# Optimization experiments

Hardware: AMD Instinct MI355X
Metric: run time of the kernel (lower is better)

The kernel has to match this reference:

```python
import jax, jax.numpy as jnp
import numpy as np

EPS = 1e-12  # matches torch F.normalize eps


def _l2norm(t):
    n = jnp.linalg.norm(t, axis=-1, keepdims=True)
    return t / jnp.maximum(n, EPS)


def setup_inputs() -> dict:
    key = jax.random.key(0)
    ks = jax.random.split(key, 10)
    B, N, C = 2, 2048, 384
    nH, hd = 12, 32
    inp = {
        "x": jax.random.normal(ks[0], (B, N, C), jnp.float32),
        "q_w": jax.random.normal(ks[1], (C, C), jnp.float32) * 0.02,
        "q_b": jax.random.normal(ks[2], (C,), jnp.float32) * 0.02,
        "kv_w": jax.random.normal(ks[3], (2 * C, C), jnp.float32) * 0.02,
        "kv_b": jax.random.normal(ks[4], (2 * C,), jnp.float32) * 0.02,
        "query_embedding": jax.random.normal(ks[5], (nH, 1, hd), jnp.float32) * 0.02,
        # init of temperature in torch: log(exp(1/0.24) - 1)
        "temperature": jnp.full((nH, 1, 1), float(np.log(np.exp(1.0 / 0.24) - 1.0)), jnp.float32),
        "pos_bias": jax.random.normal(ks[7], (nH, N), jnp.float32) * 0.0004,
        "proj_w": jax.random.normal(ks[8], (C, C), jnp.float32) * 0.02,
        "proj_b": jax.random.normal(ks[9], (C,), jnp.float32) * 0.02,
        "D": 8, "H": 16, "W": 16,
    }
    return inp


def reference(x, q_w, q_b, kv_w, kv_b, query_embedding, temperature, pos_bias, proj_w, proj_b, D, H, W):
    B, N, C = x.shape
    nH, hd = query_embedding.shape[0], query_embedding.shape[2]
    assert N == D * H * W
    # q projection -> [B, nH, N, hd], cosine-normalized
    q = (x @ q_w.T + q_b).reshape(B, N, nH, hd).transpose(0, 2, 1, 3)
    q = _l2norm(q)
    # additive query embedding, softplus temperature, seq-length (log N) scale
    scale = jax.nn.softplus(temperature) * jnp.float32(np.log(N))  # [nH,1,1]
    q = (q + query_embedding[None]) * scale[None]
    # kv projection
    kv = x @ kv_w.T + kv_b  # [B, N, 2C]
    k, v = kv[..., :C], kv[..., C:]
    k = _l2norm(k.reshape(B, N, nH, hd).transpose(0, 2, 1, 3))
    v = v.reshape(B, N, nH, hd).transpose(0, 2, 1, 3)
    # scores with per-head learned positional bias over keys
    attn = jnp.einsum("bhqd,bhkd->bhqk", q, k) + pos_bias[None, :, None, :]
    attn = jax.nn.softmax(attn, axis=-1)
    out = jnp.einsum("bhqk,bhkd->bhqd", attn, v)
    out = out.transpose(0, 2, 1, 3).reshape(B, N, C)
    return out @ proj_w.T + proj_b
```

## Files before the change

kernel.cpp:

```cpp
#include <hip/hip_runtime.h>

#define LOG2E 1.4426950408889634f

typedef __bf16 bf16x8 __attribute__((ext_vector_type(8)));
typedef short s16x4 __attribute__((ext_vector_type(4)));
typedef float f32x4 __attribute__((ext_vector_type(4)));

#define BB 2
#define NN 2048
#define CC 384
#define NH 12
#define HD 32
#define MROWS (BB * NN)

__device__ __forceinline__ unsigned short f2bf(float f) {
  __bf16 h = (__bf16)f;
  return __builtin_bit_cast(unsigned short, h);
}

__device__ __forceinline__ bf16x8 ldg_bf8(const unsigned short* p) {
  uint4 v = *reinterpret_cast<const uint4*>(p);
  return __builtin_bit_cast(bf16x8, v);
}

__device__ __forceinline__ float fexp2(float x) {
#if __has_builtin(__builtin_amdgcn_exp2f)
  return __builtin_amdgcn_exp2f(x);
#else
  return exp2f(x);
#endif
}

__device__ __forceinline__ s16x4 pack_bf4(float a, float b, float c, float d) {
#if __has_builtin(__builtin_amdgcn_cvt_pk_bf16_f32)
  auto lo = __builtin_amdgcn_cvt_pk_bf16_f32(a, b);
  auto hi = __builtin_amdgcn_cvt_pk_bf16_f32(c, d);
  uint2 u = {__builtin_bit_cast(unsigned int, lo),
             __builtin_bit_cast(unsigned int, hi)};
  return __builtin_bit_cast(s16x4, u);
#else
  s16x4 r = {(short)f2bf(a), (short)f2bf(b), (short)f2bf(c), (short)f2bf(d)};
  return r;
#endif
}

typedef __attribute__((address_space(1))) const void gas_void;
typedef __attribute__((address_space(3))) void las_void;
__device__ __forceinline__ void gload_lds16(const void* g, void* l) {
  __builtin_amdgcn_global_load_lds((gas_void*)(unsigned long long)g,
                                   (las_void*)(unsigned long long)l, 16, 0, 0);
}

__device__ __forceinline__ f32x4 mfma32(bf16x8 a, bf16x8 b, f32x4 c) {
  return __builtin_amdgcn_mfma_f32_16x16x32_bf16(a, b, c, 0, 0, 0);
}

__device__ __forceinline__ f32x4 mfma16(s16x4 a, s16x4 b, f32x4 c) {
#if defined(__HIP_DEVICE_COMPILE__)
#if __has_builtin(__builtin_amdgcn_mfma_f32_16x16x16bf16_1k)
  return __builtin_amdgcn_mfma_f32_16x16x16bf16_1k(a, b, c, 0, 0, 0);
#else
  asm volatile("v_mfma_f32_16x16x16_bf16 %0, %1, %2, %0"
               : "+v"(c) : "v"(a), "v"(b));
  return c;
#endif
#else
  return c;
#endif
}

__global__ __launch_bounds__(256) void prep_kernel(
    const float* __restrict__ x, const float* __restrict__ q_w,
    const float* __restrict__ kv_w, const float* __restrict__ proj_w,
    const float* __restrict__ pos_bias, unsigned short* __restrict__ xb,
    unsigned short* __restrict__ qwb, unsigned short* __restrict__ kvwb,
    unsigned short* __restrict__ pwb, float* __restrict__ bias2) {
  long i = (long)(blockIdx.x * 256 + threadIdx.x) * 8;
  auto cast8 = [&](const float* s, unsigned short* d, long off) {
    float4 a = *reinterpret_cast<const float4*>(s + off);
    float4 b = *reinterpret_cast<const float4*>(s + off + 4);
    s16x4 lo = pack_bf4(a.x, a.y, a.z, a.w);
    s16x4 hi = pack_bf4(b.x, b.y, b.z, b.w);
    uint2 l = __builtin_bit_cast(uint2, lo), h = __builtin_bit_cast(uint2, hi);
    uint4 o = {l.x, l.y, h.x, h.y};
    *reinterpret_cast<uint4*>(d + off) = o;
  };
  if (i < 1572864) { cast8(x, xb, i); return; }
  i -= 1572864;
  if (i < 147456) { cast8(q_w, qwb, i); return; }
  i -= 147456;
  if (i < 294912) { cast8(kv_w, kvwb, i); return; }
  i -= 294912;
  if (i < 147456) { cast8(proj_w, pwb, i); return; }
  i -= 147456;
  float4 a = *reinterpret_cast<const float4*>(pos_bias + i);
  float4 b = *reinterpret_cast<const float4*>(pos_bias + i + 4);
  a.x *= LOG2E; a.y *= LOG2E; a.z *= LOG2E; a.w *= LOG2E;
  b.x *= LOG2E; b.y *= LOG2E; b.z *= LOG2E; b.w *= LOG2E;
  *reinterpret_cast<float4*>(bias2 + i) = a;
  *reinterpret_cast<float4*>(bias2 + i + 4) = b;
}

__global__ __launch_bounds__(256, 4) void gemm_qkv_norm_kernel(
    const unsigned short* __restrict__ xb, const unsigned short* __restrict__ qwb,
    const unsigned short* __restrict__ kvwb, const float* __restrict__ q_b,
    const float* __restrict__ kv_b, const float* __restrict__ qe,
    const float* __restrict__ temperature, unsigned short* __restrict__ Qs,
    unsigned short* __restrict__ Kn, unsigned short* __restrict__ VT) {
  __shared__ alignas(16) char smem[2][20480];
  int wave = threadIdx.x >> 6, lane = threadIdx.x & 63;
  int c = lane & 15, quad = lane >> 4;
  int h = blockIdx.y;
  int m0b = blockIdx.x * 64;
  int cid = wave * 64 + lane;

  auto stage = [&](int buf, int kk) {
    char* base = smem[buf];
#pragma unroll
    for (int j = 0; j < 2; ++j) {
      int chunk = j * 256 + cid;
      int row = chunk >> 3, e = chunk & 7;
      gload_lds16(xb + (long)(m0b + row) * CC + kk + (e ^ (row & 7)) * 8,
                  base + j * 4096 + wave * 1024);
    }
#pragma unroll
    for (int j = 0; j < 3; ++j) {
      int chunk = j * 256 + cid;
      int row = chunk >> 3, e = chunk & 7;
      const unsigned short* src;
      if (row < 32)      src = qwb + (long)(h * 32 + row) * CC;
      else if (row < 64) src = kvwb + (long)(h * 32 + (row - 32)) * CC;
      else               src = kvwb + (long)(CC + h * 32 + (row - 64)) * CC;
      gload_lds16(src + kk + (e ^ (row & 7)) * 8,
                  base + 8192 + j * 4096 + wave * 1024);
    }
  };

  f32x4 acc[6] = {};
  auto compute = [&](int buf) {
    const char* base = smem[buf];
#pragma unroll
    for (int kh = 0; kh < 2; ++kh) {
      int sa = ((kh * 4 + quad) ^ (c & 7)) * 16;
      bf16x8 a = *(const bf16x8*)(base + (wave * 16 + c) * 128 + sa);
#pragma unroll
      for (int t = 0; t < 6; ++t) {
        bf16x8 b = *(const bf16x8*)(base + 8192 + (t * 16 + c) * 128 + sa);
        acc[t] = mfma32(a, b, acc[t]);
      }
    }
  };

  stage(0, 0);
#pragma unroll 1
  for (int s = 0; s < 6; ++s) {
    __syncthreads();
    if (s < 5) stage((s + 1) & 1, (s + 1) * 64);
    compute(s & 1);
  }

  int m0 = m0b + wave * 16;
  float qb0 = q_b[h * 32 + c], qb1 = q_b[h * 32 + 16 + c];
  float kb0 = kv_b[h * 32 + c], kb1 = kv_b[h * 32 + 16 + c];
  float vb0 = kv_b[CC + h * 32 + c], vb1 = kv_b[CC + h * 32 + 16 + c];
  float qe0 = qe[h * HD + c], qe1 = qe[h * HD + 16 + c];
  float sc = log1pf(expf(temperature[h])) * 11.0f;
  int b = m0 >> 11;
  int nb = (m0 & 2047) + quad * 4;
  int pair = b * NH + h;
  unsigned short* qsb = Qs + ((long)pair * NN + nb) * HD;
  unsigned short* knb = Kn + ((long)pair * NN + nb) * HD;
  ushort4 vp0, vp1;
#pragma unroll
  for (int r = 0; r < 4; ++r) {
    float q0 = acc[0][r] + qb0, q1 = acc[1][r] + qb1;
    float k0 = acc[2][r] + kb0, k1 = acc[3][r] + kb1;
    float v0 = acc[4][r] + vb0, v1 = acc[5][r] + vb1;
    float qs = q0 * q0 + q1 * q1, ks = k0 * k0 + k1 * k1;
#pragma unroll
    for (int off = 8; off; off >>= 1) {
      qs += __shfl_xor(qs, off);
      ks += __shfl_xor(ks, off);
    }
    float qi = 1.0f / fmaxf(sqrtf(qs), 1e-12f);
    float ki = 1.0f / fmaxf(sqrtf(ks), 1e-12f);
    qsb[r * HD + c] = f2bf((q0 * qi + qe0) * sc);
    qsb[r * HD + 16 + c] = f2bf((q1 * qi + qe1) * sc);
    knb[r * HD + c] = f2bf(k0 * ki);
    knb[r * HD + 16 + c] = f2bf(k1 * ki);
    ((unsigned short*)&vp0)[r] = f2bf(v0);
    ((unsigned short*)&vp1)[r] = f2bf(v1);
  }
  *reinterpret_cast<ushort4*>(VT + ((long)pair * HD + c) * NN + nb) = vp0;
  *reinterpret_cast<ushort4*>(VT + ((long)pair * HD + 16 + c) * NN + nb) = vp1;
}

__global__ __launch_bounds__(256, 4) void attn_kernel(
    const unsigned short* __restrict__ Qs, const unsigned short* __restrict__ Kn,
    const unsigned short* __restrict__ VT, const float* __restrict__ bias2,
    unsigned short* __restrict__ ao) {
  __shared__ alignas(16) char smem[2][16384];
  __shared__ alignas(16) char biasl[8192];
  int wave = threadIdx.x >> 6, lane = threadIdx.x & 63;
  int c = lane & 15, quad = lane >> 4;
  int id = blockIdx.x;
  int xcd = id & 7, rr = id >> 3;
  int pair = (rr >> 5) * 8 + xcd;
  int qt = rr & 31;
  int h = pair % NH, b = pair / NH;
  const unsigned short* Qp = Qs + (long)pair * NN * HD;
  const char* Kg0 = (const char*)(Kn + (long)pair * NN * HD);
  const char* Vg0 = (const char*)(VT + (long)pair * HD * NN);
  const char* bp = (const char*)(bias2 + h * NN);
  int q0 = qt * 64 + wave * 16;
  bf16x8 qf = ldg_bf8(Qp + (long)(q0 + c) * HD + quad * 8);
  f32x4 o0 = {}, o1 = {};
  float rs = 0.f;

  const int koff = (c * 4 + quad) * 16;

  auto stage = [&](int buf, int i) {
    char* tb = smem[buf];
    long krow0 = (long)i * 128;
    const char* Kg = Kg0 + krow0 * (HD * 2);
    const char* Vg = Vg0 + krow0 * 2;
#pragma unroll
    for (int j = 0; j < 2; ++j) {
      int ck = wave * 2 + j;
      gload_lds16(Kg + ck * 1024 + koff, tb + ck * 1024);
      int chunk = ck * 64 + lane;
      int d = chunk >> 4, e = chunk & 15;
      int es = e ^ (d & 15);
      gload_lds16(Vg + (long)d * (NN * 2) + es * 16, tb + 8192 + ck * 1024);
    }
  };

  auto compute = [&](int buf, int i) {
    const char* kb = smem[buf] + lane * 16;
    const char* vb = smem[buf] + 8192;
    const char* bl = biasl + i * 512 + quad * 16;
#pragma unroll
    for (int t8 = 0; t8 < 8; ++t8) {
      bf16x8 kf = *(const bf16x8*)(kb + t8 * 1024);
      f32x4 bbv = *(const f32x4*)(bl + t8 * 64);
      f32x4 s = mfma32(kf, qf, bbv);
      float p0 = fexp2(s[0]);
      float p1 = fexp2(s[1]);
      float p2 = fexp2(s[2]);
      float p3 = fexp2(s[3]);
      rs += (p0 + p1) + (p2 + p3);
      s16x4 pf = pack_bf4(p0, p1, p2, p3);
      int vsw = (((t8 * 2 + (quad >> 1)) ^ c) * 16) + (quad & 1) * 8;
      s16x4 vlo = *(const s16x4*)(vb + c * 256 + vsw);
      s16x4 vhi = *(const s16x4*)(vb + (c + 16) * 256 + vsw);
      o0 = mfma16(vlo, pf, o0);
      o1 = mfma16(vhi, pf, o1);
    }
  };

#pragma unroll
  for (int j = 0; j < 2; ++j)
    gload_lds16(bp + j * 4096 + wave * 1024 + lane * 16,
                biasl + j * 4096 + wave * 1024);
  stage(0, 0);
#pragma unroll 1
  for (int i = 0; i < 16; ++i) {
    __syncthreads();
    if (i < 15) stage((i + 1) & 1, i + 1);
    compute(i & 1, i);
  }

  rs += __shfl_xor(rs, 16);
  rs += __shfl_xor(rs, 32);
  float inv = 1.0f / rs;
  unsigned short* op = ao + (long)(b * NN + q0 + c) * CC + h * HD + quad * 4;
  ushort4 s0, s1;
#pragma unroll
  for (int r = 0; r < 4; ++r) {
    ((unsigned short*)&s0)[r] = f2bf(o0[r] * inv);
    ((unsigned short*)&s1)[r] = f2bf(o1[r] * inv);
  }
  *reinterpret_cast<ushort4*>(op) = s0;
  *reinterpret_cast<ushort4*>(op + 16) = s1;
}

__global__ __launch_bounds__(256, 4) void proj_kernel(
    const unsigned short* __restrict__ ab, const unsigned short* __restrict__ pwb,
    const float* __restrict__ proj_b, float* __restrict__ out) {
  __shared__ alignas(16) char smem[2][12288];
  int wave = threadIdx.x >> 6, lane = threadIdx.x & 63;
  int c = lane & 15, quad = lane >> 4;
  int m0b = blockIdx.x * 64;
  int n0 = blockIdx.y * 32;
  int cid = wave * 64 + lane;

  auto stage = [&](int buf, int kk) {
    char* base = smem[buf];
#pragma unroll
    for (int j = 0; j < 2; ++j) {
      int chunk = j * 256 + cid;
      int row = chunk >> 3, e = chunk & 7;
      gload_lds16(ab + (long)(m0b + row) * CC + kk + (e ^ (row & 7)) * 8,
                  base + j * 4096 + wave * 1024);
    }
    {
      int row = cid >> 3, e = cid & 7;
      gload_lds16(pwb + (long)(n0 + row) * CC + kk + (e ^ (row & 7)) * 8,
                  base + 8192 + wave * 1024);
    }
  };

  f32x4 acc[2] = {};
  auto compute = [&](int buf) {
    const char* base = smem[buf];
#pragma unroll
    for (int kh = 0; kh < 2; ++kh) {
      int sa = ((kh * 4 + quad) ^ (c & 7)) * 16;
      bf16x8 a = *(const bf16x8*)(base + (wave * 16 + c) * 128 + sa);
#pragma unroll
      for (int t = 0; t < 2; ++t) {
        bf16x8 b = *(const bf16x8*)(base + 8192 + (t * 16 + c) * 128 + sa);
        acc[t] = mfma32(a, b, acc[t]);
      }
    }
  };

  stage(0, 0);
#pragma unroll 1
  for (int s = 0; s < 6; ++s) {
    __syncthreads();
    if (s < 5) stage((s + 1) & 1, (s + 1) * 64);
    compute(s & 1);
  }

  int m0 = m0b + wave * 16;
#pragma unroll
  for (int t = 0; t < 2; ++t) {
    int o = n0 + t * 16 + c;
    float bv = proj_b[o];
#pragma unroll
    for (int r = 0; r < 4; ++r) {
      out[(long)(m0 + quad * 4 + r) * CC + o] = acc[t][r] + bv;
    }
  }
}

extern "C" void kernel_launch(void* const* d_in, const int* in_sizes, int n_in,
                              void* d_out, int out_size, void* d_ws, size_t ws_size,
                              hipStream_t stream) {
  const float* x = (const float*)d_in[0];
  const float* q_w = (const float*)d_in[1];
  const float* q_b = (const float*)d_in[2];
  const float* kv_w = (const float*)d_in[3];
  const float* kv_b = (const float*)d_in[4];
  const float* qe = (const float*)d_in[5];
  const float* temp = (const float*)d_in[6];
  const float* pos_bias = (const float*)d_in[7];
  const float* proj_w = (const float*)d_in[8];
  const float* proj_b = (const float*)d_in[9];
  float* out = (float*)d_out;

  char* ws = (char*)d_ws;
  unsigned short* xb = (unsigned short*)(ws + 0);
  unsigned short* qwb = (unsigned short*)(ws + 3145728);
  unsigned short* kvwb = (unsigned short*)(ws + 3440640);
  unsigned short* pwb = (unsigned short*)(ws + 4030464);
  unsigned short* Qs = (unsigned short*)(ws + 4325376);
  unsigned short* Kn = (unsigned short*)(ws + 7471104);
  unsigned short* VT = (unsigned short*)(ws + 10616832);
  unsigned short* ao = (unsigned short*)(ws + 13762560);
  float* bias2 = (float*)(ws + 16908288);

  prep_kernel<<<1068, 256, 0, stream>>>(x, q_w, kv_w, proj_w, pos_bias, xb, qwb,
                                        kvwb, pwb, bias2);
  gemm_qkv_norm_kernel<<<dim3(64, NH), 256, 0, stream>>>(xb, qwb, kvwb, q_b, kv_b,
                                                         qe, temp, Qs, Kn, VT);
  attn_kernel<<<768, 256, 0, stream>>>(Qs, Kn, VT, bias2, ao);
  proj_kernel<<<dim3(64, 12), 256, 0, stream>>>(ao, pwb, proj_b, out);
}
```

Measured before the change: 124.9 us.

## Process two query tiles per wave in attention to reuse K/V LDS fragments

```diff
diff --git a/kernel.cpp b/kernel.cpp
--- a/kernel.cpp
+++ b/kernel.cpp
@@ -195,7 +195,7 @@
   *reinterpret_cast<ushort4*>(VT + ((long)pair * HD + 16 + c) * NN + nb) = vp1;
 }
 
-__global__ __launch_bounds__(256, 4) void attn_kernel(
+__global__ __launch_bounds__(128, 2) void attn_kernel(
     const unsigned short* __restrict__ Qs, const unsigned short* __restrict__ Kn,
     const unsigned short* __restrict__ VT, const float* __restrict__ bias2,
     unsigned short* __restrict__ ao) {
@@ -212,10 +212,11 @@
   const char* Kg0 = (const char*)(Kn + (long)pair * NN * HD);
   const char* Vg0 = (const char*)(VT + (long)pair * HD * NN);
   const char* bp = (const char*)(bias2 + h * NN);
-  int q0 = qt * 64 + wave * 16;
-  bf16x8 qf = ldg_bf8(Qp + (long)(q0 + c) * HD + quad * 8);
-  f32x4 o0 = {}, o1 = {};
-  float rs = 0.f;
+  int q0 = qt * 64 + wave * 32;
+  bf16x8 qfA = ldg_bf8(Qp + (long)(q0 + c) * HD + quad * 8);
+  bf16x8 qfB = ldg_bf8(Qp + (long)(q0 + 16 + c) * HD + quad * 8);
+  f32x4 o0A = {}, o1A = {}, o0B = {}, o1B = {};
+  float rsA = 0.f, rsB = 0.f;
 
   const int koff = (c * 4 + quad) * 16;
 
@@ -225,8 +226,8 @@
     const char* Kg = Kg0 + krow0 * (HD * 2);
     const char* Vg = Vg0 + krow0 * 2;
 #pragma unroll
-    for (int j = 0; j < 2; ++j) {
-      int ck = wave * 2 + j;
+    for (int j = 0; j < 4; ++j) {
+      int ck = wave * 4 + j;
       gload_lds16(Kg + ck * 1024 + koff, tb + ck * 1024);
       int chunk = ck * 64 + lane;
       int d = chunk >> 4, e = chunk & 15;
@@ -243,25 +244,30 @@
     for (int t8 = 0; t8 < 8; ++t8) {
       bf16x8 kf = *(const bf16x8*)(kb + t8 * 1024);
       f32x4 bbv = *(const f32x4*)(bl + t8 * 64);
-      f32x4 s = mfma32(kf, qf, bbv);
-      float p0 = fexp2(s[0]);
-      float p1 = fexp2(s[1]);
-      float p2 = fexp2(s[2]);
-      float p3 = fexp2(s[3]);
-      rs += (p0 + p1) + (p2 + p3);
-      s16x4 pf = pack_bf4(p0, p1, p2, p3);
+      f32x4 sA = mfma32(kf, qfA, bbv);
+      f32x4 sB = mfma32(kf, qfB, bbv);
+      float a0 = fexp2(sA[0]), a1 = fexp2(sA[1]);
+      float a2 = fexp2(sA[2]), a3 = fexp2(sA[3]);
+      float e0 = fexp2(sB[0]), e1 = fexp2(sB[1]);
+      float e2 = fexp2(sB[2]), e3 = fexp2(sB[3]);
+      rsA += (a0 + a1) + (a2 + a3);
+      rsB += (e0 + e1) + (e2 + e3);
+      s16x4 pfA = pack_bf4(a0, a1, a2, a3);
+      s16x4 pfB = pack_bf4(e0, e1, e2, e3);
       int vsw = (((t8 * 2 + (quad >> 1)) ^ c) * 16) + (quad & 1) * 8;
       s16x4 vlo = *(const s16x4*)(vb + c * 256 + vsw);
       s16x4 vhi = *(const s16x4*)(vb + (c + 16) * 256 + vsw);
-      o0 = mfma16(vlo, pf, o0);
-      o1 = mfma16(vhi, pf, o1);
-    }
-  };
-
-#pragma unroll
-  for (int j = 0; j < 2; ++j)
-    gload_lds16(bp + j * 4096 + wave * 1024 + lane * 16,
-                biasl + j * 4096 + wave * 1024);
+      o0A = mfma16(vlo, pfA, o0A);
+      o1A = mfma16(vhi, pfA, o1A);
+      o0B = mfma16(vlo, pfB, o0B);
+      o1B = mfma16(vhi, pfB, o1B);
+    }
+  };
+
+#pragma unroll
+  for (int j = 0; j < 4; ++j)
+    gload_lds16(bp + wave * 4096 + j * 1024 + lane * 16,
+                biasl + wave * 4096 + j * 1024);
   stage(0, 0);
 #pragma unroll 1
   for (int i = 0; i < 16; ++i) {
@@ -270,18 +276,26 @@
     compute(i & 1, i);
   }
 
-  rs += __shfl_xor(rs, 16);
-  rs += __shfl_xor(rs, 32);
-  float inv = 1.0f / rs;
-  unsigned short* op = ao + (long)(b * NN + q0 + c) * CC + h * HD + quad * 4;
-  ushort4 s0, s1;
+  rsA += __shfl_xor(rsA, 16);
+  rsA += __shfl_xor(rsA, 32);
+  rsB += __shfl_xor(rsB, 16);
+  rsB += __shfl_xor(rsB, 32);
+  float invA = 1.0f / rsA;
+  float invB = 1.0f / rsB;
+  unsigned short* opA = ao + (long)(b * NN + q0 + c) * CC + h * HD + quad * 4;
+  unsigned short* opB = ao + (long)(b * NN + q0 + 16 + c) * CC + h * HD + quad * 4;
+  ushort4 sa0, sa1, sb0, sb1;
 #pragma unroll
   for (int r = 0; r < 4; ++r) {
-    ((unsigned short*)&s0)[r] = f2bf(o0[r] * inv);
-    ((unsigned short*)&s1)[r] = f2bf(o1[r] * inv);
-  }
-  *reinterpret_cast<ushort4*>(op) = s0;
-  *reinterpret_cast<ushort4*>(op + 16) = s1;
+    ((unsigned short*)&sa0)[r] = f2bf(o0A[r] * invA);
+    ((unsigned short*)&sa1)[r] = f2bf(o1A[r] * invA);
+    ((unsigned short*)&sb0)[r] = f2bf(o0B[r] * invB);
+    ((unsigned short*)&sb1)[r] = f2bf(o1B[r] * invB);
+  }
+  *reinterpret_cast<ushort4*>(opA) = sa0;
+  *reinterpret_cast<ushort4*>(opA + 16) = sa1;
+  *reinterpret_cast<ushort4*>(opB) = sb0;
+  *reinterpret_cast<ushort4*>(opB + 16) = sb1;
 }
 
 __global__ __launch_bounds__(256, 4) void proj_kernel(
@@ -375,6 +389,6 @@
                                         kvwb, pwb, bias2);
   gemm_qkv_norm_kernel<<<dim3(64, NH), 256, 0, stream>>>(xb, qwb, kvwb, q_b, kv_b,
                                                          qe, temp, Qs, Kn, VT);
-  attn_kernel<<<768, 256, 0, stream>>>(Qs, Kn, VT, bias2, ao);
+  attn_kernel<<<768, 128, 0, stream>>>(Qs, Kn, VT, bias2, ao);
   proj_kernel<<<dim3(64, 12), 256, 0, stream>>>(ao, pwb, proj_b, out);
 }
```

New measurement: 130.5 us. +4.5%, slower.
